# Optimization experiments

Hardware: AMD Instinct MI355X
Metric: run time of the kernel (lower is better)

## Reference

```python
import jax, jax.numpy as jnp
import numpy as np

DIM = 768
HEADS = 12
DIM_HEAD = 64
INNER = HEADS * DIM_HEAD  # 768
EPS = 1e-5


def setup_inputs() -> dict:
    key = jax.random.key(0)
    ks = jax.random.split(key, 5)
    x = jax.random.normal(ks[0], (8, 4096, DIM), dtype=jnp.float32)
    # nn.Linear(dim, 3*inner, bias=False): weight [3*inner, dim]
    w_map = jax.random.normal(ks[1], (3 * INNER, DIM), dtype=jnp.float32) * (1.0 / np.sqrt(DIM))
    # LayerNorm affine params over dim_head
    g_k = jnp.ones((DIM_HEAD,), dtype=jnp.float32)
    b_k = jnp.zeros((DIM_HEAD,), dtype=jnp.float32)
    g_v = jnp.ones((DIM_HEAD,), dtype=jnp.float32)
    b_v = jnp.zeros((DIM_HEAD,), dtype=jnp.float32)
    # nn.Linear(inner, dim): weight [dim, inner], bias [dim]
    w_out = jax.random.normal(ks[2], (DIM, INNER), dtype=jnp.float32) * (1.0 / np.sqrt(INNER))
    b_out = jax.random.normal(ks[3], (DIM,), dtype=jnp.float32) * 0.01
    return {"x": x, "w_map": w_map, "g_k": g_k, "b_k": b_k,
            "g_v": g_v, "b_v": b_v, "w_out": w_out, "b_out": b_out}


def _layernorm(t, gamma, beta):
    mu = jnp.mean(t, axis=-1, keepdims=True)
    var = jnp.var(t, axis=-1, keepdims=True)
    return (t - mu) * jax.lax.rsqrt(var + EPS) * gamma + beta


def reference(x, w_map, g_k, b_k, g_v, b_v, w_out, b_out):
    b, n, _ = x.shape
    qkv = x @ w_map.T  # [b, n, 3*inner]
    q, k, v = jnp.split(qkv, 3, axis=-1)
    # b n (h d) -> b h n d
    def to_heads(t):
        return t.reshape(b, n, HEADS, DIM_HEAD).transpose(0, 2, 1, 3)
    q, k, v = to_heads(q), to_heads(k), to_heads(v)
    k = _layernorm(k, g_k, b_k)
    v = _layernorm(v, g_v, b_v)
    # linear attention: context = k^T v / n, out = q @ context
    attn = jnp.einsum('bhnd,bhne->bhde', k, v) / n  # [b, h, d, d]
    out = jnp.einsum('bhnd,bhde->bhne', q, attn)    # [b, h, n, d]
    out = out.transpose(0, 2, 1, 3).reshape(b, n, INNER)
    return out @ w_out.T + b_out
```

## Files before the change

### kernel.cpp

```cpp
#include <hip/hip_runtime.h>


typedef _Float16 f16;
typedef __attribute__((ext_vector_type(4))) _Float16 f16x4;
typedef __attribute__((ext_vector_type(8))) _Float16 f16x8;
typedef __attribute__((ext_vector_type(4))) float f32x4;

#define MFMA_F16(a, b, c) __builtin_amdgcn_mfma_f32_16x16x32_f16((a), (b), (c), 0, 0, 0)

#define BATCH  8
#define NSEQ   4096
#define DIM    768
#define HEADS  12
#define DH     64
#define KOFF   768
#define VOFF   1536
#define EPS    1e-5f

#define SWZ(row, byte) ((row) * 128 + ((byte) ^ (((row) & 7) << 4)))
#define SWZ256(row, byte) ((row) * 256 + ((byte) ^ (((row) & 7) << 4)))

__device__ __forceinline__ void gl16(const void* g, void* l) {
    __builtin_amdgcn_global_load_lds(
        (const __attribute__((address_space(1))) void*)g,
        (__attribute__((address_space(3))) void*)l, 16, 0, 0);
}

__global__ void convert_kernel(const float* __restrict__ src,
                               f16* __restrict__ dst, size_t n8)
{
    size_t i = (size_t)blockIdx.x * blockDim.x + threadIdx.x;
    size_t stride = (size_t)gridDim.x * blockDim.x;
    for (; i < n8; i += stride) {
        const float4* s = (const float4*)(src + i * 8);
        float4 v0 = s[0], v1 = s[1];
        f16x8 h = { (f16)v0.x, (f16)v0.y, (f16)v0.z, (f16)v0.w,
                    (f16)v1.x, (f16)v1.y, (f16)v1.z, (f16)v1.w };
        *(f16x8*)(dst + i * 8) = h;
    }
}

__global__ void transp_q_kernel(const float* __restrict__ w_map,
                                f16* __restrict__ whqT)
{
    __shared__ f16 tl[64][80];
    const int tid = threadIdx.x;
    const int hd0 = blockIdx.x * 64, c0 = blockIdx.y * 64;
    #pragma unroll
    for (int t = 0; t < 4; ++t) {
        int idx = tid + t * 256;
        int r = idx >> 4, c4 = (idx & 15) << 2;
        float4 v = *(const float4*)(w_map + (size_t)(hd0 + r) * DIM + c0 + c4);
        tl[c4 + 0][r] = (f16)v.x;
        tl[c4 + 1][r] = (f16)v.y;
        tl[c4 + 2][r] = (f16)v.z;
        tl[c4 + 3][r] = (f16)v.w;
    }
    __syncthreads();
    #pragma unroll
    for (int t = 0; t < 2; ++t) {
        int idx = tid + t * 256;
        int c = idx >> 3, p = idx & 7;
        f16x8 hv = *(f16x8*)&tl[c][p * 8];
        *(f16x8*)(whqT + (size_t)(c0 + c) * DIM + hd0 + p * 8) = hv;
    }
}

__launch_bounds__(256, 2)
__global__ void kv_ctx_kernel(const f16* __restrict__ xh,
                              const f16* __restrict__ wh,
                              const float* __restrict__ g_k,
                              const float* __restrict__ b_k,
                              const float* __restrict__ g_v,
                              const float* __restrict__ b_v,
                              float* __restrict__ ctx)
{
    __shared__ __align__(16) char smem[32768];

    const int tid  = threadIdx.x;
    const int lane = tid & 63;
    const int w    = tid >> 6;
    const int wr   = w >> 1;
    const int wc   = w & 1;
    const int l15  = lane & 15;
    const int hi   = lane >> 4;
    const int lr   = lane >> 3;
    const int lb   = (lane & 7) << 4;
    const int srcB = lb ^ (lr << 4);
    const int n0   = blockIdx.x * 128;
    const int h    = blockIdx.y;
    const int bb   = blockIdx.z;

    const char* px = (const char*)xh
        + ((size_t)(bb * NSEQ + n0 + w * 32 + lr) * DIM) * 2 + srcB;
    const int kvr  = w * 32 + lr;
    const int wrow = (kvr < DH) ? (KOFF + h * DH + kvr) : (VOFF + h * DH + kvr - DH);
    const char* pw = (const char*)wh + ((size_t)wrow * DIM) * 2 + srcB;
    char* dxb = smem + w * 4096;
    char* dwb = smem + 16384 + w * 4096;

    f32x4 acc[4][4];
    #pragma unroll
    for (int m = 0; m < 4; ++m)
        #pragma unroll
        for (int n = 0; n < 4; ++n)
            acc[m][n] = (f32x4)(0.f);

    for (int c0 = 0; c0 < DIM; c0 += 64) {
        __syncthreads();
        const int kbyt = c0 * 2;
        #pragma unroll
        for (int i = 0; i < 4; ++i) {
            gl16(px + kbyt + i * 12288, dxb + i * 1024);
            gl16(pw + kbyt + i * 12288, dwb + i * 1024);
        }
        __syncthreads();
        #pragma unroll
        for (int kk = 0; kk < 2; ++kk) {
            const int kb = (kk * 32 + hi * 8) * 2;
            f16x8 a[4], b[4];
            #pragma unroll
            for (int m = 0; m < 4; ++m) {
                int row = wr * 64 + m * 16 + l15;
                a[m] = *(const f16x8*)(smem + SWZ(row, kb));
            }
            #pragma unroll
            for (int n = 0; n < 4; ++n) {
                int col = wc * 64 + n * 16 + l15;
                b[n] = *(const f16x8*)(smem + 16384 + SWZ(col, kb));
            }
            #pragma unroll
            for (int m = 0; m < 4; ++m)
                #pragma unroll
                for (int n = 0; n < 4; ++n)
                    acc[m][n] = MFMA_F16(a[m], b[n], acc[m][n]);
        }
    }
    __syncthreads();

    const float* gp = wc ? g_v : g_k;
    const float* bp = wc ? b_v : b_k;
    float gg[4], be[4];
    #pragma unroll
    for (int n = 0; n < 4; ++n) { gg[n] = gp[n * 16 + l15]; be[n] = bp[n * 16 + l15]; }

    char* tbuf = smem + wc * 16384;

    #pragma unroll
    for (int m = 0; m < 4; ++m) {
        float o[4][4];
        #pragma unroll
        for (int r = 0; r < 4; ++r) {
            float s = 0.f, ss = 0.f;
            #pragma unroll
            for (int n = 0; n < 4; ++n) { float t = acc[m][n][r]; s += t; ss += t * t; }
            s += __shfl_xor(s, 1); ss += __shfl_xor(ss, 1);
            s += __shfl_xor(s, 2); ss += __shfl_xor(ss, 2);
            s += __shfl_xor(s, 4); ss += __shfl_xor(ss, 4);
            s += __shfl_xor(s, 8); ss += __shfl_xor(ss, 8);
            float mu  = s * (1.f / DH);
            float var = ss * (1.f / DH) - mu * mu;
            float rs  = rsqrtf(var + EPS);
            #pragma unroll
            for (int n = 0; n < 4; ++n)
                o[r][n] = (acc[m][n][r] - mu) * rs * gg[n] + be[n];
        }
        const int nrow0 = wr * 64 + m * 16 + hi * 4;
        #pragma unroll
        for (int n = 0; n < 4; ++n) {
            int col = n * 16 + l15;
            f16x4 hv = { (f16)o[0][n], (f16)o[1][n], (f16)o[2][n], (f16)o[3][n] };
            *(f16x4*)(tbuf + SWZ256(col, nrow0 * 2)) = hv;
        }
    }
    __syncthreads();

    f32x4 c2[4];
    #pragma unroll
    for (int e = 0; e < 4; ++e) c2[e] = (f32x4)(0.f);
    #pragma unroll
    for (int ks = 0; ks < 4; ++ks) {
        const int kb = (ks * 32 + hi * 8) * 2;
        int drow = w * 16 + l15;
        f16x8 ak = *(const f16x8*)(smem + SWZ256(drow, kb));
        #pragma unroll
        for (int e = 0; e < 4; ++e) {
            int col = e * 16 + l15;
            f16x8 bv = *(const f16x8*)(smem + 16384 + SWZ256(col, kb));
            c2[e] = MFMA_F16(ak, bv, c2[e]);
        }
    }
    float* cbase = ctx + (size_t)(bb * HEADS + h) * DH * DH;
    #pragma unroll
    for (int e = 0; e < 4; ++e)
        #pragma unroll
        for (int r = 0; r < 4; ++r) {
            int d  = w * 16 + hi * 4 + r;
            int ee = e * 16 + l15;
            atomicAdd(cbase + d * DH + ee, c2[e][r]);
        }
}

__launch_bounds__(256)
__global__ void ctx_wout_kernel(const float* __restrict__ ctx,
                                const float* __restrict__ w_out,
                                f16* __restrict__ ThT)
{
    __shared__ float cs[DH * DH];
    const int tid = threadIdx.x;
    const int jt = blockIdx.x, h = blockIdx.y, bb = blockIdx.z;
    const float scale = 1.f / NSEQ;
    const float* cbase = ctx + (size_t)(bb * HEADS + h) * DH * DH;
    for (int t = tid; t < DH * DH; t += 256) cs[t] = cbase[t] * scale;
    __syncthreads();

    const int j = jt * 256 + tid;
    float wv[DH];
    const float* wrow = w_out + (size_t)j * DIM + h * DH;
    #pragma unroll
    for (int e4 = 0; e4 < DH; e4 += 4) {
        float4 v = *(const float4*)(wrow + e4);
        wv[e4] = v.x; wv[e4 + 1] = v.y; wv[e4 + 2] = v.z; wv[e4 + 3] = v.w;
    }
    f16* trow = ThT + ((size_t)bb * DIM + j) * DIM + h * DH;
    for (int d = 0; d < DH; ++d) {
        float a = 0.f;
        #pragma unroll
        for (int e = 0; e < DH; ++e) a += cs[d * DH + e] * wv[e];
        trow[d] = (f16)a;
    }
}

__launch_bounds__(256, 2)
__global__ void fold_q_kernel(const f16* __restrict__ ThT,
                              const f16* __restrict__ whqT,
                              f16* __restrict__ WcT)
{
    __shared__ __align__(16) char smem[32768];

    const int tid  = threadIdx.x;
    const int lane = tid & 63;
    const int w    = tid >> 6;
    const int wr   = w >> 1, wc = w & 1;
    const int l15  = lane & 15, hi = lane >> 4;
    const int lr   = lane >> 3;
    const int lb   = (lane & 7) << 4;
    const int srcB = lb ^ (lr << 4);
    const int j0   = blockIdx.x * 128;
    const int c0g  = blockIdx.y * 128;
    const int bb   = blockIdx.z;

    const char* pa = (const char*)ThT
        + ((size_t)(bb * DIM + j0 + w * 32 + lr) * DIM) * 2 + srcB;
    const char* pb = (const char*)whqT
        + ((size_t)(c0g + w * 32 + lr) * DIM) * 2 + srcB;
    char* dab = smem + w * 4096;
    char* dbb = smem + 16384 + w * 4096;

    f32x4 acc[4][4];
    #pragma unroll
    for (int m = 0; m < 4; ++m)
        #pragma unroll
        for (int n = 0; n < 4; ++n)
            acc[m][n] = (f32x4)(0.f);

    for (int k0 = 0; k0 < DIM; k0 += 64) {
        __syncthreads();
        const int kbyt = k0 * 2;
        #pragma unroll
        for (int i = 0; i < 4; ++i) {
            gl16(pa + kbyt + i * 12288, dab + i * 1024);
            gl16(pb + kbyt + i * 12288, dbb + i * 1024);
        }
        __syncthreads();
        #pragma unroll
        for (int kk = 0; kk < 2; ++kk) {
            const int kb = (kk * 32 + hi * 8) * 2;
            f16x8 a[4], b[4];
            #pragma unroll
            for (int m = 0; m < 4; ++m) {
                int row = wr * 64 + m * 16 + l15;
                a[m] = *(const f16x8*)(smem + SWZ(row, kb));
            }
            #pragma unroll
            for (int n = 0; n < 4; ++n) {
                int col = wc * 64 + n * 16 + l15;
                b[n] = *(const f16x8*)(smem + 16384 + SWZ(col, kb));
            }
            #pragma unroll
            for (int m = 0; m < 4; ++m)
                #pragma unroll
                for (int n = 0; n < 4; ++n)
                    acc[m][n] = MFMA_F16(a[m], b[n], acc[m][n]);
        }
    }

    f16* ob = WcT + (size_t)bb * DIM * DIM;
    #pragma unroll
    for (int m = 0; m < 4; ++m)
        #pragma unroll
        for (int n = 0; n < 4; ++n)
            #pragma unroll
            for (int r = 0; r < 4; ++r) {
                int j = j0 + wr * 64 + m * 16 + hi * 4 + r;
                int c = c0g + wc * 64 + n * 16 + l15;
                ob[(size_t)j * DIM + c] = (f16)acc[m][n][r];
            }
}

__launch_bounds__(256, 2)
__global__ void final_gemm_kernel(const f16* __restrict__ xh,
                                  const f16* __restrict__ WcT,
                                  const float* __restrict__ b_out,
                                  float* __restrict__ out)
{
    __shared__ __align__(16) char smem[32768];

    const int tid  = threadIdx.x;
    const int lane = tid & 63;
    const int w    = tid >> 6;
    const int wr   = w >> 1, wc = w & 1;
    const int l15  = lane & 15, hi = lane >> 4;
    const int lr   = lane >> 3;
    const int lb   = (lane & 7) << 4;
    const int srcB = lb ^ (lr << 4);
    const int n0   = blockIdx.x * 128;
    const int j0   = blockIdx.y * 128;
    const int bb   = blockIdx.z;

    const char* pa = (const char*)xh
        + ((size_t)(bb * NSEQ + n0 + w * 32 + lr) * DIM) * 2 + srcB;
    const char* pb = (const char*)WcT
        + ((size_t)(bb * DIM + j0 + w * 32 + lr) * DIM) * 2 + srcB;
    char* dab = smem + w * 4096;
    char* dbb = smem + 16384 + w * 4096;

    f32x4 acc[4][4];
    #pragma unroll
    for (int m = 0; m < 4; ++m)
        #pragma unroll
        for (int n = 0; n < 4; ++n)
            acc[m][n] = (f32x4)(0.f);

    for (int c0 = 0; c0 < DIM; c0 += 64) {
        __syncthreads();
        const int kbyt = c0 * 2;
        #pragma unroll
        for (int i = 0; i < 4; ++i) {
            gl16(pa + kbyt + i * 12288, dab + i * 1024);
            gl16(pb + kbyt + i * 12288, dbb + i * 1024);
        }
        __syncthreads();
        #pragma unroll
        for (int kk = 0; kk < 2; ++kk) {
            const int kb = (kk * 32 + hi * 8) * 2;
            f16x8 a[4], b[4];
            #pragma unroll
            for (int m = 0; m < 4; ++m) {
                int row = wr * 64 + m * 16 + l15;
                a[m] = *(const f16x8*)(smem + SWZ(row, kb));
            }
            #pragma unroll
            for (int n = 0; n < 4; ++n) {
                int col = wc * 64 + n * 16 + l15;
                b[n] = *(const f16x8*)(smem + 16384 + SWZ(col, kb));
            }
            #pragma unroll
            for (int m = 0; m < 4; ++m)
                #pragma unroll
                for (int n = 0; n < 4; ++n)
                    acc[m][n] = MFMA_F16(a[m], b[n], acc[m][n]);
        }
    }

    float bias[4];
    #pragma unroll
    for (int n = 0; n < 4; ++n) bias[n] = b_out[j0 + wc * 64 + n * 16 + l15];

    float* ob = out + ((size_t)bb * NSEQ + n0) * DIM;
    #pragma unroll
    for (int m = 0; m < 4; ++m)
        #pragma unroll
        for (int n = 0; n < 4; ++n)
            #pragma unroll
            for (int r = 0; r < 4; ++r) {
                int rn = wr * 64 + m * 16 + hi * 4 + r;
                int cj = j0 + wc * 64 + n * 16 + l15;
                ob[(size_t)rn * DIM + cj] = acc[m][n][r] + bias[n];
            }
}

extern "C" void kernel_launch(void* const* d_in, const int* in_sizes, int n_in,
                              void* d_out, int out_size, void* d_ws, size_t ws_size,
                              hipStream_t stream)
{
    (void)in_sizes; (void)n_in; (void)out_size; (void)ws_size;
    const float* x     = (const float*)d_in[0];
    const float* w_map = (const float*)d_in[1];
    const float* g_k   = (const float*)d_in[2];
    const float* b_k   = (const float*)d_in[3];
    const float* g_v   = (const float*)d_in[4];
    const float* b_v   = (const float*)d_in[5];
    const float* w_out = (const float*)d_in[6];
    const float* b_out = (const float*)d_in[7];
    float* out = (float*)d_out;

    char* wsb  = (char*)d_ws;
    float* ctx = (float*)wsb;                       wsb += (size_t)BATCH * HEADS * DH * DH * 4;
    f16* xh    = (f16*)wsb;                         wsb += (size_t)BATCH * NSEQ * DIM * 2;
    f16* wh    = (f16*)wsb;                         wsb += (size_t)3 * DIM * DIM * 2;
    f16* whqT  = (f16*)wsb;                         wsb += (size_t)DIM * DIM * 2;
    f16* ThT   = (f16*)wsb;                         wsb += (size_t)BATCH * DIM * DIM * 2;
    f16* WcT   = (f16*)wsb;

    hipMemsetAsync(ctx, 0, (size_t)BATCH * HEADS * DH * DH * sizeof(float), stream);

    convert_kernel<<<2048, 256, 0, stream>>>(x, xh, (size_t)BATCH * NSEQ * DIM / 8);
    convert_kernel<<<864, 256, 0, stream>>>(w_map, wh, (size_t)3 * DIM * DIM / 8);
    dim3 gT(12, 12);
    transp_q_kernel<<<gT, 256, 0, stream>>>(w_map, whqT);

    dim3 gA(NSEQ / 128, HEADS, BATCH);
    kv_ctx_kernel<<<gA, 256, 0, stream>>>(xh, wh, g_k, b_k, g_v, b_v, ctx);

    dim3 gB1(DIM / 256, HEADS, BATCH);
    ctx_wout_kernel<<<gB1, 256, 0, stream>>>(ctx, w_out, ThT);

    dim3 gB2(DIM / 128, DIM / 128, BATCH);
    fold_q_kernel<<<gB2, 256, 0, stream>>>(ThT, whqT, WcT);

    dim3 gC(NSEQ / 128, DIM / 128, BATCH);
    final_gemm_kernel<<<gC, 256, 0, stream>>>(xh, WcT, b_out, out);
}
```

Baseline: 390.8 us.

## Widen KV-context and final GEMM tiles to 128x256 with 512-thread blocks

The KV-context kernel now handles two heads per block, and the final GEMM handles 256 output columns per block, both using 8 waves. Each 128-row x tile loaded into LDS is therefore reused across twice as many output columns, which halves how often x is re-read from global memory. The per-head LayerNorm and k^T v step is serialized into two passes that share LDS, adding extra barriers. LDS use grows to 48KB per block and the launch bounds change, which may lower occupancy.

New measurement: 449.9 us. +15.1%, slower.

```diff
diff --git a/kernel.cpp b/kernel.cpp
--- a/kernel.cpp
+++ b/kernel.cpp
@@ -66,7 +66,7 @@
     }
 }
 
-__launch_bounds__(256, 2)
+__launch_bounds__(512, 4)
 __global__ void kv_ctx_kernel(const f16* __restrict__ xh,
                               const f16* __restrict__ wh,
                               const float* __restrict__ g_k,
@@ -75,28 +75,33 @@
                               const float* __restrict__ b_v,
                               float* __restrict__ ctx)
 {
-    __shared__ __align__(16) char smem[32768];
+    __shared__ __align__(16) char smem[49152];
 
     const int tid  = threadIdx.x;
     const int lane = tid & 63;
     const int w    = tid >> 6;
-    const int wr   = w >> 1;
-    const int wc   = w & 1;
+    const int wr   = w >> 2;
+    const int wcq  = w & 3;
     const int l15  = lane & 15;
     const int hi   = lane >> 4;
     const int lr   = lane >> 3;
     const int lb   = (lane & 7) << 4;
     const int srcB = lb ^ (lr << 4);
     const int n0   = blockIdx.x * 128;
-    const int h    = blockIdx.y;
+    const int h0   = blockIdx.y * 2;
     const int bb   = blockIdx.z;
 
     const char* px = (const char*)xh
-        + ((size_t)(bb * NSEQ + n0 + w * 32 + lr) * DIM) * 2 + srcB;
-    const int kvr  = w * 32 + lr;
-    const int wrow = (kvr < DH) ? (KOFF + h * DH + kvr) : (VOFF + h * DH + kvr - DH);
-    const char* pw = (const char*)wh + ((size_t)wrow * DIM) * 2 + srcB;
-    char* dxb = smem + w * 4096;
+        + ((size_t)(bb * NSEQ + n0 + w * 16 + lr) * DIM) * 2 + srcB;
+    const char* pw[4];
+    #pragma unroll
+    for (int i = 0; i < 4; ++i) {
+        int kvr = w * 32 + i * 8 + lr;
+        int seg = kvr >> 6;
+        int wrow = ((seg & 1) ? VOFF : KOFF) + (h0 + (seg >> 1)) * DH + (kvr & 63);
+        pw[i] = (const char*)wh + ((size_t)wrow * DIM) * 2 + srcB;
+    }
+    char* dxb = smem + w * 2048;
     char* dwb = smem + 16384 + w * 4096;
 
     f32x4 acc[4][4];
@@ -110,10 +115,11 @@
         __syncthreads();
         const int kbyt = c0 * 2;
         #pragma unroll
-        for (int i = 0; i < 4; ++i) {
+        for (int i = 0; i < 2; ++i)
             gl16(px + kbyt + i * 12288, dxb + i * 1024);
-            gl16(pw + kbyt + i * 12288, dwb + i * 1024);
-        }
+        #pragma unroll
+        for (int i = 0; i < 4; ++i)
+            gl16(pw[i] + kbyt, dwb + i * 1024);
         __syncthreads();
         #pragma unroll
         for (int kk = 0; kk < 2; ++kk) {
@@ -126,8 +132,8 @@
             }
             #pragma unroll
             for (int n = 0; n < 4; ++n) {
-                int col = wc * 64 + n * 16 + l15;
-                b[n] = *(const f16x8*)(smem + 16384 + SWZ(col, kb));
+                int row = wcq * 64 + n * 16 + l15;
+                b[n] = *(const f16x8*)(smem + 16384 + SWZ(row, kb));
             }
             #pragma unroll
             for (int m = 0; m < 4; ++m)
@@ -138,67 +144,72 @@
     }
     __syncthreads();
 
-    const float* gp = wc ? g_v : g_k;
-    const float* bp = wc ? b_v : b_k;
+    const int  isv  = wcq & 1;
+    const int  myhp = wcq >> 1;
+    const float* gp = isv ? g_v : g_k;
+    const float* bp = isv ? b_v : b_k;
     float gg[4], be[4];
     #pragma unroll
     for (int n = 0; n < 4; ++n) { gg[n] = gp[n * 16 + l15]; be[n] = bp[n * 16 + l15]; }
 
-    char* tbuf = smem + wc * 16384;
-
-    #pragma unroll
-    for (int m = 0; m < 4; ++m) {
-        float o[4][4];
-        #pragma unroll
-        for (int r = 0; r < 4; ++r) {
-            float s = 0.f, ss = 0.f;
-            #pragma unroll
-            for (int n = 0; n < 4; ++n) { float t = acc[m][n][r]; s += t; ss += t * t; }
-            s += __shfl_xor(s, 1); ss += __shfl_xor(ss, 1);
-            s += __shfl_xor(s, 2); ss += __shfl_xor(ss, 2);
-            s += __shfl_xor(s, 4); ss += __shfl_xor(ss, 4);
-            s += __shfl_xor(s, 8); ss += __shfl_xor(ss, 8);
-            float mu  = s * (1.f / DH);
-            float var = ss * (1.f / DH) - mu * mu;
-            float rs  = rsqrtf(var + EPS);
-            #pragma unroll
-            for (int n = 0; n < 4; ++n)
-                o[r][n] = (acc[m][n][r] - mu) * rs * gg[n] + be[n];
-        }
-        const int nrow0 = wr * 64 + m * 16 + hi * 4;
-        #pragma unroll
-        for (int n = 0; n < 4; ++n) {
-            int col = n * 16 + l15;
-            f16x4 hv = { (f16)o[0][n], (f16)o[1][n], (f16)o[2][n], (f16)o[3][n] };
-            *(f16x4*)(tbuf + SWZ256(col, nrow0 * 2)) = hv;
-        }
-    }
-    __syncthreads();
-
-    f32x4 c2[4];
-    #pragma unroll
-    for (int e = 0; e < 4; ++e) c2[e] = (f32x4)(0.f);
-    #pragma unroll
-    for (int ks = 0; ks < 4; ++ks) {
-        const int kb = (ks * 32 + hi * 8) * 2;
-        int drow = w * 16 + l15;
-        f16x8 ak = *(const f16x8*)(smem + SWZ256(drow, kb));
-        #pragma unroll
-        for (int e = 0; e < 4; ++e) {
-            int col = e * 16 + l15;
-            f16x8 bv = *(const f16x8*)(smem + 16384 + SWZ256(col, kb));
-            c2[e] = MFMA_F16(ak, bv, c2[e]);
-        }
-    }
-    float* cbase = ctx + (size_t)(bb * HEADS + h) * DH * DH;
-    #pragma unroll
-    for (int e = 0; e < 4; ++e)
-        #pragma unroll
-        for (int r = 0; r < 4; ++r) {
-            int d  = w * 16 + hi * 4 + r;
-            int ee = e * 16 + l15;
-            atomicAdd(cbase + d * DH + ee, c2[e][r]);
-        }
+    for (int hpass = 0; hpass < 2; ++hpass) {
+        if (myhp == hpass) {
+            char* tbuf = smem + isv * 16384;
+            #pragma unroll
+            for (int m = 0; m < 4; ++m) {
+                float o[4][4];
+                #pragma unroll
+                for (int r = 0; r < 4; ++r) {
+                    float s = 0.f, ss = 0.f;
+                    #pragma unroll
+                    for (int n = 0; n < 4; ++n) { float t = acc[m][n][r]; s += t; ss += t * t; }
+                    s += __shfl_xor(s, 1); ss += __shfl_xor(ss, 1);
+                    s += __shfl_xor(s, 2); ss += __shfl_xor(ss, 2);
+                    s += __shfl_xor(s, 4); ss += __shfl_xor(ss, 4);
+                    s += __shfl_xor(s, 8); ss += __shfl_xor(ss, 8);
+                    float mu  = s * (1.f / DH);
+                    float var = ss * (1.f / DH) - mu * mu;
+                    float rs  = rsqrtf(var + EPS);
+                    #pragma unroll
+                    for (int n = 0; n < 4; ++n)
+                        o[r][n] = (acc[m][n][r] - mu) * rs * gg[n] + be[n];
+                }
+                const int nrow0 = wr * 64 + m * 16 + hi * 4;
+                #pragma unroll
+                for (int n = 0; n < 4; ++n) {
+                    int col = n * 16 + l15;
+                    f16x4 hv = { (f16)o[0][n], (f16)o[1][n], (f16)o[2][n], (f16)o[3][n] };
+                    *(f16x4*)(tbuf + SWZ256(col, nrow0 * 2)) = hv;
+                }
+            }
+        }
+        __syncthreads();
+
+        f32x4 c2[2];
+        c2[0] = (f32x4)(0.f); c2[1] = (f32x4)(0.f);
+        #pragma unroll
+        for (int ks = 0; ks < 4; ++ks) {
+            const int kb = (ks * 32 + hi * 8) * 2;
+            int drow = (w & 3) * 16 + l15;
+            f16x8 ak = *(const f16x8*)(smem + SWZ256(drow, kb));
+            #pragma unroll
+            for (int ef = 0; ef < 2; ++ef) {
+                int col = (w >> 2) * 32 + ef * 16 + l15;
+                f16x8 bv = *(const f16x8*)(smem + 16384 + SWZ256(col, kb));
+                c2[ef] = MFMA_F16(ak, bv, c2[ef]);
+            }
+        }
+        float* cbase = ctx + (size_t)(bb * HEADS + h0 + hpass) * DH * DH;
+        #pragma unroll
+        for (int ef = 0; ef < 2; ++ef)
+            #pragma unroll
+            for (int r = 0; r < 4; ++r) {
+                int d  = (w & 3) * 16 + hi * 4 + r;
+                int ee = (w >> 2) * 32 + ef * 16 + l15;
+                atomicAdd(cbase + d * DH + ee, c2[ef][r]);
+            }
+        __syncthreads();
+    }
 }
 
 __launch_bounds__(256)
@@ -308,31 +319,31 @@
             }
 }
 
-__launch_bounds__(256, 2)
+__launch_bounds__(512, 4)
 __global__ void final_gemm_kernel(const f16* __restrict__ xh,
                                   const f16* __restrict__ WcT,
                                   const float* __restrict__ b_out,
                                   float* __restrict__ out)
 {
-    __shared__ __align__(16) char smem[32768];
+    __shared__ __align__(16) char smem[49152];
 
     const int tid  = threadIdx.x;
     const int lane = tid & 63;
     const int w    = tid >> 6;
-    const int wr   = w >> 1, wc = w & 1;
+    const int wr   = w >> 2, wcq = w & 3;
     const int l15  = lane & 15, hi = lane >> 4;
     const int lr   = lane >> 3;
     const int lb   = (lane & 7) << 4;
     const int srcB = lb ^ (lr << 4);
     const int n0   = blockIdx.x * 128;
-    const int j0   = blockIdx.y * 128;
+    const int j0   = blockIdx.y * 256;
     const int bb   = blockIdx.z;
 
     const char* pa = (const char*)xh
-        + ((size_t)(bb * NSEQ + n0 + w * 32 + lr) * DIM) * 2 + srcB;
+        + ((size_t)(bb * NSEQ + n0 + w * 16 + lr) * DIM) * 2 + srcB;
     const char* pb = (const char*)WcT
         + ((size_t)(bb * DIM + j0 + w * 32 + lr) * DIM) * 2 + srcB;
-    char* dab = smem + w * 4096;
+    char* dab = smem + w * 2048;
     char* dbb = smem + 16384 + w * 4096;
 
     f32x4 acc[4][4];
@@ -346,10 +357,11 @@
         __syncthreads();
         const int kbyt = c0 * 2;
         #pragma unroll
-        for (int i = 0; i < 4; ++i) {
+        for (int i = 0; i < 2; ++i)
             gl16(pa + kbyt + i * 12288, dab + i * 1024);
+        #pragma unroll
+        for (int i = 0; i < 4; ++i)
             gl16(pb + kbyt + i * 12288, dbb + i * 1024);
-        }
         __syncthreads();
         #pragma unroll
         for (int kk = 0; kk < 2; ++kk) {
@@ -362,8 +374,8 @@
             }
             #pragma unroll
             for (int n = 0; n < 4; ++n) {
-                int col = wc * 64 + n * 16 + l15;
-                b[n] = *(const f16x8*)(smem + 16384 + SWZ(col, kb));
+                int row = wcq * 64 + n * 16 + l15;
+                b[n] = *(const f16x8*)(smem + 16384 + SWZ(row, kb));
             }
             #pragma unroll
             for (int m = 0; m < 4; ++m)
@@ -375,7 +387,7 @@
 
     float bias[4];
     #pragma unroll
-    for (int n = 0; n < 4; ++n) bias[n] = b_out[j0 + wc * 64 + n * 16 + l15];
+    for (int n = 0; n < 4; ++n) bias[n] = b_out[j0 + wcq * 64 + n * 16 + l15];
 
     float* ob = out + ((size_t)bb * NSEQ + n0) * DIM;
     #pragma unroll
@@ -385,7 +397,7 @@
             #pragma unroll
             for (int r = 0; r < 4; ++r) {
                 int rn = wr * 64 + m * 16 + hi * 4 + r;
-                int cj = j0 + wc * 64 + n * 16 + l15;
+                int cj = j0 + wcq * 64 + n * 16 + l15;
                 ob[(size_t)rn * DIM + cj] = acc[m][n][r] + bias[n];
             }
 }
@@ -420,8 +432,8 @@
     dim3 gT(12, 12);
     transp_q_kernel<<<gT, 256, 0, stream>>>(w_map, whqT);
 
-    dim3 gA(NSEQ / 128, HEADS, BATCH);
-    kv_ctx_kernel<<<gA, 256, 0, stream>>>(xh, wh, g_k, b_k, g_v, b_v, ctx);
+    dim3 gA(NSEQ / 128, HEADS / 2, BATCH);
+    kv_ctx_kernel<<<gA, 512, 0, stream>>>(xh, wh, g_k, b_k, g_v, b_v, ctx);
 
     dim3 gB1(DIM / 256, HEADS, BATCH);
     ctx_wout_kernel<<<gB1, 256, 0, stream>>>(ctx, w_out, ThT);
@@ -429,6 +441,6 @@
     dim3 gB2(DIM / 128, DIM / 128, BATCH);
     fold_q_kernel<<<gB2, 256, 0, stream>>>(ThT, whqT, WcT);
 
-    dim3 gC(NSEQ / 128, DIM / 128, BATCH);
-    final_gemm_kernel<<<gC, 256, 0, stream>>>(xh, WcT, b_out, out);
-}
+    dim3 gC(NSEQ / 128, DIM / 256, BATCH);
+    final_gemm_kernel<<<gC, 512, 0, stream>>>(xh, WcT, b_out, out);
+}
```
